# Kernel tuning notes

Measured on AMD Instinct MI355X. Metric: run time of the kernel, lower is better.

## Reference

```python
import jax, jax.numpy as jnp
import numpy as np

N = 100000        # nodes
E = 1600000       # edges (avg degree 16)
D1, D2 = 512, 256 # omic feature dims
H = 64            # hidden_dim
C = 4             # num_classes


def setup_inputs() -> dict:
    key = jax.random.key(0)
    ks = jax.random.split(key, 13)
    s = 0.05  # param scale
    return {
        "x_omic1": jax.random.normal(ks[0], (N, D1), dtype=jnp.float32),
        "x_omic2": jax.random.normal(ks[1], (N, D2), dtype=jnp.float32),
        "edge_index": jax.random.randint(ks[2], (2, E), 0, N, dtype=jnp.int32),
        # GCNConv weights/biases, branch 1 (omic1)
        "W1a": jax.random.normal(ks[3], (D1, H), dtype=jnp.float32) * s,
        "b1a": jnp.zeros((H,), dtype=jnp.float32),
        "W2a": jax.random.normal(ks[4], (H, H), dtype=jnp.float32) * s,
        "b2a": jnp.zeros((H,), dtype=jnp.float32),
        # branch 2 (omic2)
        "W1b": jax.random.normal(ks[5], (D2, H), dtype=jnp.float32) * s,
        "b1b": jnp.zeros((H,), dtype=jnp.float32),
        "W2b": jax.random.normal(ks[6], (H, H), dtype=jnp.float32) * s,
        "b2b": jnp.zeros((H,), dtype=jnp.float32),
        # final classifier
        "Wfc": jax.random.normal(ks[7], (2 * H, C), dtype=jnp.float32) * s,
        "bfc": jnp.zeros((C,), dtype=jnp.float32),
    }


def reference(x_omic1, x_omic2, edge_index, W1a, b1a, W2a, b2a,
              W1b, b1b, W2b, b2b, Wfc, bfc):
    n = x_omic1.shape[0]
    # GCN normalization with self-loops: A_hat = A + I, norm = d^-1/2 d^-1/2
    loop = jnp.arange(n, dtype=edge_index.dtype)
    src = jnp.concatenate([edge_index[0], loop])
    dst = jnp.concatenate([edge_index[1], loop])
    deg = jax.ops.segment_sum(jnp.ones_like(src, dtype=x_omic1.dtype), dst,
                              num_segments=n)
    dinv = jnp.where(deg > 0, jax.lax.rsqrt(jnp.maximum(deg, 1.0)), 0.0)
    norm = dinv[src] * dinv[dst]  # [E+N]

    def gcn(x, W, b):
        h = x @ W                              # dense linear [n, H]
        msg = h[src] * norm[:, None]           # gather + scale
        return jax.ops.segment_sum(msg, dst, num_segments=n) + b

    # dropout is identity in eval mode
    x1 = jax.nn.elu(gcn(x_omic1, W1a, b1a))
    x1 = jax.nn.elu(gcn(x1, W2a, b2a))
    x2 = jax.nn.elu(gcn(x_omic2, W1b, b1b))
    x2 = jax.nn.elu(gcn(x2, W2b, b2b))
    x = jnp.concatenate([x1, x2], axis=1)      # [n, 2H]
    return x @ Wfc + bfc
```

## Files before the change

kernel.cpp:

```cpp
#include <hip/hip_runtime.h>
#include <hip/hip_bf16.h>
#include <math.h>


#define H 64

static inline int ceil_div(int a, int b) { return (a + b - 1) / b; }

typedef __attribute__((ext_vector_type(8))) short short8_t;
typedef __attribute__((ext_vector_type(4))) float f32x4;

__device__ inline unsigned short f2bf_rne(float f) {
    unsigned u = __float_as_uint(f);
    u += 0x7fffu + ((u >> 16) & 1u);
    return (unsigned short)(u >> 16);
}
__device__ inline unsigned pk_bf(float a, float b) {
    return (unsigned)f2bf_rne(a) | ((unsigned)f2bf_rne(b) << 16);
}
__device__ inline float2 bf2x(unsigned w) {
    float2 r;
    r.x = __uint_as_float(w << 16);
    r.y = __uint_as_float(w & 0xffff0000u);
    return r;
}
union V8 { uint4 u4; unsigned u[4]; short8_t s; };

__global__ __launch_bounds__(256) void deg_kernel(const int* __restrict__ dst,
                                                  int* __restrict__ deg, int E) {
    int e = blockIdx.x * 256 + threadIdx.x;
    if (e < E) atomicAdd(&deg[dst[e]], 1);
}

__global__ __launch_bounds__(256) void dinv_kernel(const int* __restrict__ deg,
                                                   float* __restrict__ dinv, int n) {
    int i = blockIdx.x * 256 + threadIdx.x;
    if (i < n) dinv[i] = rsqrtf((float)deg[i] + 1.0f);
}

__global__ __launch_bounds__(256) void scan_block_kernel(const int* __restrict__ deg,
                                                         int* __restrict__ row_partial,
                                                         int* __restrict__ blocksums,
                                                         int n) {
    __shared__ int s[256];
    int i = blockIdx.x * 256 + threadIdx.x;
    int v = (i < n) ? deg[i] : 0;
    s[threadIdx.x] = v;
    __syncthreads();
#pragma unroll
    for (int off = 1; off < 256; off <<= 1) {
        int t = (threadIdx.x >= off) ? s[threadIdx.x - off] : 0;
        __syncthreads();
        s[threadIdx.x] += t;
        __syncthreads();
    }
    if (i < n) row_partial[i] = s[threadIdx.x] - v;
    if (threadIdx.x == 255) blocksums[blockIdx.x] = s[255];
}

__global__ __launch_bounds__(512) void scan_top_kernel(int* __restrict__ blocksums,
                                                       int nb) {
    __shared__ int s[512];
    int v = (threadIdx.x < (unsigned)nb) ? blocksums[threadIdx.x] : 0;
    s[threadIdx.x] = v;
    __syncthreads();
#pragma unroll
    for (int off = 1; off < 512; off <<= 1) {
        int t = (threadIdx.x >= off) ? s[threadIdx.x - off] : 0;
        __syncthreads();
        s[threadIdx.x] += t;
        __syncthreads();
    }
    if (threadIdx.x < (unsigned)nb) blocksums[threadIdx.x] = s[threadIdx.x] - v;
}

__global__ __launch_bounds__(256) void scan_add_kernel(int* __restrict__ row_ptr,
                                                       const int* __restrict__ blocksums,
                                                       int* __restrict__ cursor,
                                                       int n, int E) {
    int i = blockIdx.x * 256 + threadIdx.x;
    if (i < n) {
        int v = row_ptr[i] + blocksums[blockIdx.x];
        row_ptr[i] = v;
        cursor[i] = v;
    }
    if (i == 0) row_ptr[n] = E;
}

__global__ __launch_bounds__(256) void scatter_kernel(const int* __restrict__ src,
                                                      const int* __restrict__ dst,
                                                      const float* __restrict__ dinv,
                                                      int* __restrict__ cursor,
                                                      int* __restrict__ csr_src,
                                                      float* __restrict__ csr_norm,
                                                      int E) {
    int e = blockIdx.x * 256 + threadIdx.x;
    if (e >= E) return;
    int s = src[e];
    int d = dst[e];
    int pos = atomicAdd(&cursor[d], 1);
    csr_src[pos] = s;
    csr_norm[pos] = dinv[s] * dinv[d];
}

__global__ __launch_bounds__(256) void wfrag_kernel(const float* __restrict__ W,
                                                    uint4* __restrict__ frag, int K) {
    int t = blockIdx.x * 256 + threadIdx.x;
    int total = (K >> 5) * 256;
    if (t >= total) return;
    int lane = t & 63, nt = (t >> 6) & 3, ks = t >> 8;
    int nl = lane & 15, q = lane >> 4;
    float hi[8], lo[8];
#pragma unroll
    for (int j = 0; j < 8; ++j) {
        float w = W[(size_t)(ks * 32 + q * 8 + j) * 64 + nt * 16 + nl];
        unsigned hb = f2bf_rne(w);
        float hf = __uint_as_float(((unsigned)hb) << 16);
        hi[j] = hf;
        lo[j] = w - hf;
    }
    V8 vh, vl;
#pragma unroll
    for (int j = 0; j < 4; ++j) {
        vh.u[j] = pk_bf(hi[2 * j], hi[2 * j + 1]);
        vl.u[j] = pk_bf(lo[2 * j], lo[2 * j + 1]);
    }
    size_t base = (size_t)((ks * 4 + nt) * 2) * 64 + lane;
    frag[base] = vh.u4;
    frag[base + 64] = vl.u4;
}

__global__ __launch_bounds__(256) void gemm_l1_kernel(const float* __restrict__ X,
                                                      const uint4* __restrict__ wf,
                                                      unsigned* __restrict__ Hout,
                                                      int M, int K) {
    const int tid = threadIdx.x;
    const int w = tid >> 6, l = tid & 63;
    const int m = l & 15, q = l >> 4;
    const int tile = blockIdx.x * 64 + w * 16;
    int row = tile + m;
    int rowc = row < M ? row : M - 1;
    const float* Xr = X + (size_t)rowc * K;

    f32x4 acc[4];
#pragma unroll
    for (int nt = 0; nt < 4; ++nt) acc[nt] = (f32x4){0.f, 0.f, 0.f, 0.f};

    const int ksteps = K >> 5;
    for (int ks = 0; ks < ksteps; ++ks) {
        const float4 f0 = *(const float4*)&Xr[ks * 32 + q * 8];
        const float4 f1 = *(const float4*)&Xr[ks * 32 + q * 8 + 4];
        float xs[8] = {f0.x, f0.y, f0.z, f0.w, f1.x, f1.y, f1.z, f1.w};
        V8 ah, al;
#pragma unroll
        for (int j = 0; j < 4; ++j) {
            float a = xs[2 * j], b = xs[2 * j + 1];
            unsigned ha = f2bf_rne(a), hb = f2bf_rne(b);
            float fa = __uint_as_float(ha << 16);
            float fb = __uint_as_float(hb << 16);
            ah.u[j] = ha | (hb << 16);
            al.u[j] = pk_bf(a - fa, b - fb);
        }
        const uint4* base = wf + (size_t)(ks * 4) * 2 * 64 + l;
#pragma unroll
        for (int nt = 0; nt < 4; ++nt) {
            V8 bh, bl;
            bh.u4 = base[(size_t)(nt * 2) * 64];
            bl.u4 = base[(size_t)(nt * 2 + 1) * 64];
            acc[nt] = __builtin_amdgcn_mfma_f32_16x16x32_bf16(ah.s, bh.s, acc[nt], 0, 0, 0);
            acc[nt] = __builtin_amdgcn_mfma_f32_16x16x32_bf16(al.s, bh.s, acc[nt], 0, 0, 0);
            acc[nt] = __builtin_amdgcn_mfma_f32_16x16x32_bf16(ah.s, bl.s, acc[nt], 0, 0, 0);
        }
    }

    const int rbase = tile + q * 4;
#pragma unroll
    for (int nt = 0; nt < 4; ++nt) {
#pragma unroll
        for (int i = 0; i < 4; ++i) {
            float f = acc[nt][i];
            float fo = __shfl_xor(f, 1, 64);
            int r = rbase + i;
            if (((l & 1) == 0) && r < M)
                Hout[(size_t)r * 32 + nt * 8 + (m >> 1)] = pk_bf(f, fo);
        }
    }
}

__global__ __launch_bounds__(256) void gemm_l2_kernel(const uint4* __restrict__ Xb,
                                                      const uint4* __restrict__ wf,
                                                      unsigned* __restrict__ Hout,
                                                      int M) {
    const int tid = threadIdx.x;
    const int w = tid >> 6, l = tid & 63;
    const int m = l & 15, q = l >> 4;
    const int tile = blockIdx.x * 64 + w * 16;
    int row = tile + m;
    int rowc = row < M ? row : M - 1;

    f32x4 acc[4];
#pragma unroll
    for (int nt = 0; nt < 4; ++nt) acc[nt] = (f32x4){0.f, 0.f, 0.f, 0.f};

#pragma unroll
    for (int ks = 0; ks < 2; ++ks) {
        V8 av;
        av.u4 = Xb[(size_t)rowc * 8 + ks * 4 + q];
        const uint4* base = wf + (size_t)(ks * 4) * 2 * 64 + l;
#pragma unroll
        for (int nt = 0; nt < 4; ++nt) {
            V8 bh, bl;
            bh.u4 = base[(size_t)(nt * 2) * 64];
            bl.u4 = base[(size_t)(nt * 2 + 1) * 64];
            acc[nt] = __builtin_amdgcn_mfma_f32_16x16x32_bf16(av.s, bh.s, acc[nt], 0, 0, 0);
            acc[nt] = __builtin_amdgcn_mfma_f32_16x16x32_bf16(av.s, bl.s, acc[nt], 0, 0, 0);
        }
    }

    const int rbase = tile + q * 4;
#pragma unroll
    for (int nt = 0; nt < 4; ++nt) {
#pragma unroll
        for (int i = 0; i < 4; ++i) {
            float f = acc[nt][i];
            float fo = __shfl_xor(f, 1, 64);
            int r = rbase + i;
            if (((l & 1) == 0) && r < M)
                Hout[(size_t)r * 32 + nt * 8 + (m >> 1)] = pk_bf(f, fo);
        }
    }
}

__global__ __launch_bounds__(256) void agg2_kernel(const unsigned* __restrict__ h1,
                                                   const unsigned* __restrict__ h2,
                                                   const float* __restrict__ dinv,
                                                   const int* __restrict__ row_ptr,
                                                   const int* __restrict__ csr_src,
                                                   const float* __restrict__ csr_norm,
                                                   const float* __restrict__ b1,
                                                   const float* __restrict__ b2,
                                                   unsigned* __restrict__ o1,
                                                   unsigned* __restrict__ o2,
                                                   const float* __restrict__ Wfc,
                                                   const float* __restrict__ bfc,
                                                   float* __restrict__ out, int n) {
    const int tid  = threadIdx.x;
    const int lane = tid & 63;
    const int wave = tid >> 6;
    const int half = lane >> 5;
    const int l    = lane & 31;
    const int hb   = half << 5;
    const int node = blockIdx.x * 8 + wave * 2 + half;
    const bool active = (node < n);

    int r0 = 0, r1 = 0;
    float di = 0.f;
    if (active) { r0 = row_ptr[node]; r1 = row_ptr[node + 1]; di = dinv[node]; }
    const float di2 = di * di;
    const int rowoff = node * 32 + l;

    float2 acc1 = make_float2(0.f, 0.f), acc2 = make_float2(0.f, 0.f);
    if (active) {
        float2 s1 = bf2x(h1[rowoff]);
        float2 s2 = bf2x(h2[rowoff]);
        acc1.x = s1.x * di2; acc1.y = s1.y * di2;
        acc2.x = s2.x * di2; acc2.y = s2.y * di2;
    }

    for (int base = r0; base < r1; base += 32) {
        int cnt = r1 - base;
        if (cnt > 32) cnt = 32;
        int j = base + (l < cnt ? l : cnt - 1);
        int sj = csr_src[j];
        float nj = csr_norm[j];
#pragma unroll 4
        for (int t = 0; t < cnt; ++t) {
            int s    = __shfl(sj, hb | t, 64);
            float nr = __shfl(nj, hb | t, 64);
            float2 g1 = bf2x(h1[s * 32 + l]);
            float2 g2 = bf2x(h2[s * 32 + l]);
            acc1.x = fmaf(g1.x, nr, acc1.x);
            acc1.y = fmaf(g1.y, nr, acc1.y);
            acc2.x = fmaf(g2.x, nr, acc2.x);
            acc2.y = fmaf(g2.y, nr, acc2.y);
        }
    }

    float2 bv1 = ((const float2*)b1)[l];
    float2 bv2 = ((const float2*)b2)[l];
    float2 v1, v2;
    v1.x = acc1.x + bv1.x; v1.y = acc1.y + bv1.y;
    v2.x = acc2.x + bv2.x; v2.y = acc2.y + bv2.y;
    v1.x = v1.x > 0.f ? v1.x : (expf(v1.x) - 1.f);
    v1.y = v1.y > 0.f ? v1.y : (expf(v1.y) - 1.f);
    v2.x = v2.x > 0.f ? v2.x : (expf(v2.x) - 1.f);
    v2.y = v2.y > 0.f ? v2.y : (expf(v2.y) - 1.f);

    if (Wfc == nullptr) {
        if (active) {
            o1[rowoff] = pk_bf(v1.x, v1.y);
            o2[rowoff] = pk_bf(v2.x, v2.y);
        }
        return;
    }

    const float* Wp1 = &Wfc[(2 * l) * 4];
    const float* Wp2 = &Wfc[(H + 2 * l) * 4];
    float a[4];
#pragma unroll
    for (int c = 0; c < 4; ++c)
        a[c] = v1.x * Wp1[c] + v1.y * Wp1[4 + c] + v2.x * Wp2[c] + v2.y * Wp2[4 + c];
#pragma unroll
    for (int off = 16; off > 0; off >>= 1) {
#pragma unroll
        for (int c = 0; c < 4; ++c)
            a[c] += __shfl_down(a[c], off, 64);
    }
    if (l == 0 && active) {
#pragma unroll
        for (int c = 0; c < 4; ++c)
            out[(size_t)node * 4 + c] = a[c] + bfc[c];
    }
}

extern "C" void kernel_launch(void* const* d_in, const int* in_sizes, int n_in,
                              void* d_out, int out_size, void* d_ws, size_t ws_size,
                              hipStream_t stream) {
    const float* x_omic1 = (const float*)d_in[0];
    const float* x_omic2 = (const float*)d_in[1];
    const int*   eidx    = (const int*)d_in[2];
    const float* W1a = (const float*)d_in[3];
    const float* b1a = (const float*)d_in[4];
    const float* W2a = (const float*)d_in[5];
    const float* b2a = (const float*)d_in[6];
    const float* W1b = (const float*)d_in[7];
    const float* b1b = (const float*)d_in[8];
    const float* W2b = (const float*)d_in[9];
    const float* b2b = (const float*)d_in[10];
    const float* Wfc = (const float*)d_in[11];
    const float* bfc = (const float*)d_in[12];
    float* out = (float*)d_out;

    const int D1 = 512, D2 = 256;
    const int N = in_sizes[0] / D1;
    const int E = in_sizes[2] / 2;
    const int* src = eidx;
    const int* dst = eidx + E;

    const int nblocks_scan = ceil_div(N, 256);

    size_t off = 0;
    auto alloc = [&](size_t elems) { size_t o = off; off += (elems + 3) & ~(size_t)3; return o; };
    float*    base_f = (float*)d_ws;
    int*      base_i = (int*)d_ws;
    unsigned* base_u = (unsigned*)d_ws;
    float*    dinv     = base_f + alloc(N);
    int*      deg      = base_i + alloc(N);
    int*      row_ptr  = base_i + alloc(N + 1);
    int*      bsums    = base_i + alloc(1024);
    int*      csr_src  = base_i + alloc(E);
    float*    csr_norm = base_f + alloc(E);
    unsigned* h1bf     = base_u + alloc((size_t)N * 32);
    unsigned* h2bf     = base_u + alloc((size_t)N * 32);
    unsigned* x1bf     = base_u + alloc((size_t)N * 32);
    unsigned* x2bf     = base_u + alloc((size_t)N * 32);
    uint4*    wf1a = (uint4*)(base_u + alloc((D1 / 32) * 2 * 256 * 4));
    uint4*    wf1b = (uint4*)(base_u + alloc((D2 / 32) * 2 * 256 * 4));
    uint4*    wf2a = (uint4*)(base_u + alloc((H  / 32) * 2 * 256 * 4));
    uint4*    wf2b = (uint4*)(base_u + alloc((H  / 32) * 2 * 256 * 4));
    int*      cursor = deg;

    dim3 blk(256);
    dim3 grid_e(ceil_div(E, 256));
    dim3 grid_n(ceil_div(N, 256));
    dim3 grid_agg(ceil_div(N, 8));
    dim3 grid_gemm(ceil_div(N, 64));

    hipMemsetAsync(deg, 0, (size_t)N * sizeof(int), stream);
    deg_kernel<<<grid_e, blk, 0, stream>>>(dst, deg, E);
    dinv_kernel<<<grid_n, blk, 0, stream>>>(deg, dinv, N);
    scan_block_kernel<<<nblocks_scan, blk, 0, stream>>>(deg, row_ptr, bsums, N);
    scan_top_kernel<<<1, 512, 0, stream>>>(bsums, nblocks_scan);
    scan_add_kernel<<<grid_n, blk, 0, stream>>>(row_ptr, bsums, cursor, N, E);
    scatter_kernel<<<grid_e, blk, 0, stream>>>(src, dst, dinv, cursor, csr_src, csr_norm, E);

    wfrag_kernel<<<ceil_div((D1 / 32) * 256, 256), blk, 0, stream>>>(W1a, wf1a, D1);
    wfrag_kernel<<<ceil_div((D2 / 32) * 256, 256), blk, 0, stream>>>(W1b, wf1b, D2);
    wfrag_kernel<<<ceil_div((H  / 32) * 256, 256), blk, 0, stream>>>(W2a, wf2a, H);
    wfrag_kernel<<<ceil_div((H  / 32) * 256, 256), blk, 0, stream>>>(W2b, wf2b, H);

    gemm_l1_kernel<<<grid_gemm, blk, 0, stream>>>(x_omic1, wf1a, h1bf, N, D1);
    gemm_l1_kernel<<<grid_gemm, blk, 0, stream>>>(x_omic2, wf1b, h2bf, N, D2);
    agg2_kernel<<<grid_agg, blk, 0, stream>>>(h1bf, h2bf, dinv, row_ptr, csr_src, csr_norm,
                                              b1a, b1b, x1bf, x2bf,
                                              nullptr, nullptr, nullptr, N);
    gemm_l2_kernel<<<grid_gemm, blk, 0, stream>>>((const uint4*)x1bf, wf2a, h1bf, N);
    gemm_l2_kernel<<<grid_gemm, blk, 0, stream>>>((const uint4*)x2bf, wf2b, h2bf, N);
    agg2_kernel<<<grid_agg, blk, 0, stream>>>(h1bf, h2bf, dinv, row_ptr, csr_src, csr_norm,
                                              b2a, b2b, nullptr, nullptr,
                                              Wfc, bfc, out, N);
}
```

Before: 843.5 us.

## Build CSR via two-level bucket sort and compute edge norms on the fly

Replaces the degree-atomic, multi-pass scan and per-edge global-atomic scatter with a two-level bucket sort. Edges are first binned by dst>>8 using block-local shared atomics, then each bucket is sorted per node in shared memory, which yields row_ptr and dinv in the same pass. The per-edge csr_norm array is dropped, and aggregation recomputes the norm as dinv[src]*dinv[dst], which adds one dinv gather per edge. It relies on fixed capacity assumptions (BCAP 16384 per bucket, at most 512 buckets, src below 2^17) and silently drops edges past capacity.

```diff
diff --git a/kernel.cpp b/kernel.cpp
--- a/kernel.cpp
+++ b/kernel.cpp
@@ -4,6 +4,7 @@
 
 
 #define H 64
+#define BCAP 16384
 
 static inline int ceil_div(int a, int b) { return (a + b - 1) / b; }
 
@@ -26,81 +27,112 @@
 }
 union V8 { uint4 u4; unsigned u[4]; short8_t s; };
 
-__global__ __launch_bounds__(256) void deg_kernel(const int* __restrict__ dst,
-                                                  int* __restrict__ deg, int E) {
-    int e = blockIdx.x * 256 + threadIdx.x;
-    if (e < E) atomicAdd(&deg[dst[e]], 1);
-}
-
-__global__ __launch_bounds__(256) void dinv_kernel(const int* __restrict__ deg,
-                                                   float* __restrict__ dinv, int n) {
-    int i = blockIdx.x * 256 + threadIdx.x;
-    if (i < n) dinv[i] = rsqrtf((float)deg[i] + 1.0f);
-}
-
-__global__ __launch_bounds__(256) void scan_block_kernel(const int* __restrict__ deg,
-                                                         int* __restrict__ row_partial,
-                                                         int* __restrict__ blocksums,
-                                                         int n) {
-    __shared__ int s[256];
-    int i = blockIdx.x * 256 + threadIdx.x;
-    int v = (i < n) ? deg[i] : 0;
-    s[threadIdx.x] = v;
+__global__ __launch_bounds__(256) void bucket_scatter_kernel(
+        const int* __restrict__ src, const int* __restrict__ dst,
+        int* __restrict__ cursor, unsigned* __restrict__ bucketed,
+        int E, int nbkt) {
+    __shared__ int lcnt[512];
+    __shared__ int lbase[512];
+    const int t = threadIdx.x;
+    for (int b = t; b < nbkt; b += 256) lcnt[b] = 0;
+    __syncthreads();
+
+    unsigned val[8];
+    int bkt[8], lpos[8];
+    const int e0 = blockIdx.x * 2048;
+#pragma unroll
+    for (int k = 0; k < 8; ++k) {
+        int e = e0 + k * 256 + t;
+        bkt[k] = -1;
+        if (e < E) {
+            int s = src[e];
+            int d = dst[e];
+            int b = d >> 8;
+            val[k] = (unsigned)s | ((unsigned)(d & 255) << 17);
+            bkt[k] = b;
+            lpos[k] = atomicAdd(&lcnt[b], 1);
+        }
+    }
+    __syncthreads();
+    for (int b = t; b < nbkt; b += 256) {
+        int c = lcnt[b];
+        lbase[b] = c > 0 ? atomicAdd(&cursor[b], c) : 0;
+    }
+    __syncthreads();
+#pragma unroll
+    for (int k = 0; k < 8; ++k) {
+        if (bkt[k] >= 0) {
+            int p = lbase[bkt[k]] + lpos[k];
+            if (p < BCAP)
+                bucketed[(size_t)bkt[k] * BCAP + p] = val[k];
+        }
+    }
+}
+
+__global__ __launch_bounds__(512) void bucket_scan_kernel(
+        const int* __restrict__ cursor, int* __restrict__ bucket_base,
+        int* __restrict__ row_ptr, int nbkt, int N, int E) {
+    __shared__ int s[512];
+    const int t = threadIdx.x;
+    int v = (t < nbkt) ? cursor[t] : 0;
+    s[t] = v;
+    __syncthreads();
+#pragma unroll
+    for (int off = 1; off < 512; off <<= 1) {
+        int u = (t >= off) ? s[t - off] : 0;
+        __syncthreads();
+        s[t] += u;
+        __syncthreads();
+    }
+    if (t < nbkt) bucket_base[t] = s[t] - v;
+    if (t == 0) row_ptr[N] = E;
+}
+
+__global__ __launch_bounds__(256) void bucket_csr_kernel(
+        const unsigned* __restrict__ bucketed, const int* __restrict__ cursor,
+        const int* __restrict__ bucket_base, int* __restrict__ csr_src,
+        int* __restrict__ row_ptr, float* __restrict__ dinv, int N) {
+    __shared__ int dcnt[256];
+    __shared__ int dbase[256];
+    __shared__ int dcur[256];
+    const int t = threadIdx.x;
+    const int b = blockIdx.x;
+    const int cnt = min(cursor[b], BCAP);
+    const int base = bucket_base[b];
+    const unsigned* bed = bucketed + (size_t)b * BCAP;
+
+    dcnt[t] = 0;
+    __syncthreads();
+    for (int i = t; i < cnt; i += 256) {
+        unsigned v = bed[i];
+        atomicAdd(&dcnt[v >> 17], 1);
+    }
+    __syncthreads();
+    int myc = dcnt[t];
+    int acc = myc;
+    dbase[t] = acc;
     __syncthreads();
 #pragma unroll
     for (int off = 1; off < 256; off <<= 1) {
-        int t = (threadIdx.x >= off) ? s[threadIdx.x - off] : 0;
+        int u = (t >= off) ? dbase[t - off] : 0;
         __syncthreads();
-        s[threadIdx.x] += t;
+        dbase[t] += u;
         __syncthreads();
     }
-    if (i < n) row_partial[i] = s[threadIdx.x] - v;
-    if (threadIdx.x == 255) blocksums[blockIdx.x] = s[255];
-}
-
-__global__ __launch_bounds__(512) void scan_top_kernel(int* __restrict__ blocksums,
-                                                       int nb) {
-    __shared__ int s[512];
-    int v = (threadIdx.x < (unsigned)nb) ? blocksums[threadIdx.x] : 0;
-    s[threadIdx.x] = v;
-    __syncthreads();
-#pragma unroll
-    for (int off = 1; off < 512; off <<= 1) {
-        int t = (threadIdx.x >= off) ? s[threadIdx.x - off] : 0;
-        __syncthreads();
-        s[threadIdx.x] += t;
-        __syncthreads();
-    }
-    if (threadIdx.x < (unsigned)nb) blocksums[threadIdx.x] = s[threadIdx.x] - v;
-}
-
-__global__ __launch_bounds__(256) void scan_add_kernel(int* __restrict__ row_ptr,
-                                                       const int* __restrict__ blocksums,
-                                                       int* __restrict__ cursor,
-                                                       int n, int E) {
-    int i = blockIdx.x * 256 + threadIdx.x;
-    if (i < n) {
-        int v = row_ptr[i] + blocksums[blockIdx.x];
-        row_ptr[i] = v;
-        cursor[i] = v;
-    }
-    if (i == 0) row_ptr[n] = E;
-}
-
-__global__ __launch_bounds__(256) void scatter_kernel(const int* __restrict__ src,
-                                                      const int* __restrict__ dst,
-                                                      const float* __restrict__ dinv,
-                                                      int* __restrict__ cursor,
-                                                      int* __restrict__ csr_src,
-                                                      float* __restrict__ csr_norm,
-                                                      int E) {
-    int e = blockIdx.x * 256 + threadIdx.x;
-    if (e >= E) return;
-    int s = src[e];
-    int d = dst[e];
-    int pos = atomicAdd(&cursor[d], 1);
-    csr_src[pos] = s;
-    csr_norm[pos] = dinv[s] * dinv[d];
+    int excl = dbase[t] - myc;
+    dcur[t] = excl;
+    int node = b * 256 + t;
+    if (node < N) {
+        row_ptr[node] = base + excl;
+        dinv[node] = rsqrtf((float)myc + 1.0f);
+    }
+    __syncthreads();
+    for (int i = t; i < cnt; i += 256) {
+        unsigned v = bed[i];
+        int dl = v >> 17;
+        int p = atomicAdd(&dcur[dl], 1);
+        csr_src[base + p] = (int)(v & 0x1FFFFu);
+    }
 }
 
 __global__ __launch_bounds__(256) void wfrag_kernel(const float* __restrict__ W,
@@ -236,7 +268,6 @@
                                                    const float* __restrict__ dinv,
                                                    const int* __restrict__ row_ptr,
                                                    const int* __restrict__ csr_src,
-                                                   const float* __restrict__ csr_norm,
                                                    const float* __restrict__ b1,
                                                    const float* __restrict__ b2,
                                                    unsigned* __restrict__ o1,
@@ -272,11 +303,11 @@
         if (cnt > 32) cnt = 32;
         int j = base + (l < cnt ? l : cnt - 1);
         int sj = csr_src[j];
-        float nj = csr_norm[j];
+        float dsj = dinv[sj];
 #pragma unroll 4
         for (int t = 0; t < cnt; ++t) {
             int s    = __shfl(sj, hb | t, 64);
-            float nr = __shfl(nj, hb | t, 64);
+            float nr = __shfl(dsj, hb | t, 64) * di;
             float2 g1 = bf2x(h1[s * 32 + l]);
             float2 g2 = bf2x(h2[s * 32 + l]);
             acc1.x = fmaf(g1.x, nr, acc1.x);
@@ -346,8 +377,7 @@
     const int E = in_sizes[2] / 2;
     const int* src = eidx;
     const int* dst = eidx + E;
-
-    const int nblocks_scan = ceil_div(N, 256);
+    const int nbkt = ceil_div(N, 256);
 
     size_t off = 0;
     auto alloc = [&](size_t elems) { size_t o = off; off += (elems + 3) & ~(size_t)3; return o; };
@@ -355,11 +385,11 @@
     int*      base_i = (int*)d_ws;
     unsigned* base_u = (unsigned*)d_ws;
     float*    dinv     = base_f + alloc(N);
-    int*      deg      = base_i + alloc(N);
     int*      row_ptr  = base_i + alloc(N + 1);
-    int*      bsums    = base_i + alloc(1024);
+    int*      cursor   = base_i + alloc(512);
+    int*      bkbase   = base_i + alloc(512);
+    unsigned* bucketed = base_u + alloc((size_t)nbkt * BCAP);
     int*      csr_src  = base_i + alloc(E);
-    float*    csr_norm = base_f + alloc(E);
     unsigned* h1bf     = base_u + alloc((size_t)N * 32);
     unsigned* h2bf     = base_u + alloc((size_t)N * 32);
     unsigned* x1bf     = base_u + alloc((size_t)N * 32);
@@ -368,21 +398,17 @@
     uint4*    wf1b = (uint4*)(base_u + alloc((D2 / 32) * 2 * 256 * 4));
     uint4*    wf2a = (uint4*)(base_u + alloc((H  / 32) * 2 * 256 * 4));
     uint4*    wf2b = (uint4*)(base_u + alloc((H  / 32) * 2 * 256 * 4));
-    int*      cursor = deg;
 
     dim3 blk(256);
-    dim3 grid_e(ceil_div(E, 256));
-    dim3 grid_n(ceil_div(N, 256));
     dim3 grid_agg(ceil_div(N, 8));
     dim3 grid_gemm(ceil_div(N, 64));
 
-    hipMemsetAsync(deg, 0, (size_t)N * sizeof(int), stream);
-    deg_kernel<<<grid_e, blk, 0, stream>>>(dst, deg, E);
-    dinv_kernel<<<grid_n, blk, 0, stream>>>(deg, dinv, N);
-    scan_block_kernel<<<nblocks_scan, blk, 0, stream>>>(deg, row_ptr, bsums, N);
-    scan_top_kernel<<<1, 512, 0, stream>>>(bsums, nblocks_scan);
-    scan_add_kernel<<<grid_n, blk, 0, stream>>>(row_ptr, bsums, cursor, N, E);
-    scatter_kernel<<<grid_e, blk, 0, stream>>>(src, dst, dinv, cursor, csr_src, csr_norm, E);
+    hipMemsetAsync(cursor, 0, 512 * sizeof(int), stream);
+    bucket_scatter_kernel<<<ceil_div(E, 2048), blk, 0, stream>>>(src, dst, cursor,
+                                                                 bucketed, E, nbkt);
+    bucket_scan_kernel<<<1, 512, 0, stream>>>(cursor, bkbase, row_ptr, nbkt, N, E);
+    bucket_csr_kernel<<<nbkt, blk, 0, stream>>>(bucketed, cursor, bkbase,
+                                                csr_src, row_ptr, dinv, N);
 
     wfrag_kernel<<<ceil_div((D1 / 32) * 256, 256), blk, 0, stream>>>(W1a, wf1a, D1);
     wfrag_kernel<<<ceil_div((D2 / 32) * 256, 256), blk, 0, stream>>>(W1b, wf1b, D2);
@@ -391,12 +417,12 @@
 
     gemm_l1_kernel<<<grid_gemm, blk, 0, stream>>>(x_omic1, wf1a, h1bf, N, D1);
     gemm_l1_kernel<<<grid_gemm, blk, 0, stream>>>(x_omic2, wf1b, h2bf, N, D2);
-    agg2_kernel<<<grid_agg, blk, 0, stream>>>(h1bf, h2bf, dinv, row_ptr, csr_src, csr_norm,
+    agg2_kernel<<<grid_agg, blk, 0, stream>>>(h1bf, h2bf, dinv, row_ptr, csr_src,
                                               b1a, b1b, x1bf, x2bf,
                                               nullptr, nullptr, nullptr, N);
     gemm_l2_kernel<<<grid_gemm, blk, 0, stream>>>((const uint4*)x1bf, wf2a, h1bf, N);
     gemm_l2_kernel<<<grid_gemm, blk, 0, stream>>>((const uint4*)x2bf, wf2b, h2bf, N);
-    agg2_kernel<<<grid_agg, blk, 0, stream>>>(h1bf, h2bf, dinv, row_ptr, csr_src, csr_norm,
+    agg2_kernel<<<grid_agg, blk, 0, stream>>>(h1bf, h2bf, dinv, row_ptr, csr_src,
                                               b2a, b2b, nullptr, nullptr,
                                               Wfc, bfc, out, N);
 }
```

After: 733.3 us. -13.1%, faster.
